# Performance work log

Hardware: AMD Instinct MI355X
Metric: run time of the kernel (lower is better)

Reference implementation:

```python
import jax, jax.numpy as jnp
import numpy as np

B, N, D, H, L = 16, 1024, 256, 128, 2  # batch, nodes, feat dim, gcn_hidden, n_layers (D == 2*H)


def setup_inputs() -> dict:
    key = jax.random.key(0)
    ks = jax.random.split(key, 16)
    inp = {
        "gcn_input": jax.random.normal(ks[0], (B, N, D), jnp.float32),
        # scale adjacencies by 1/N so aggregated features stay O(1)
        "latent_adj": jax.random.uniform(ks[1], (B, N, N), jnp.float32) / N,
        "dep_adj": jax.random.uniform(ks[2], (B, N, N), jnp.float32) / N,
        # stacked per-layer parameters (leading dim L); layers share shapes since D == 2*H
        "refine_gate": jax.random.normal(ks[3], (L, D, 1), jnp.float32) * 0.02,
        "gate_W_in": jax.random.normal(ks[4], (L, D, 1), jnp.float32) * 0.02,
        "gate_b_in": jnp.zeros((L, 1), jnp.float32),
        "gate_W_out": jax.random.normal(ks[5], (L, D, 1), jnp.float32) * 0.02,
        "gate_b_out": jnp.zeros((L, 1), jnp.float32),
        "fc_in_W": jax.random.normal(ks[6], (L, H, D), jnp.float32) * 0.02,
        "fc_in_b": jnp.zeros((L, H), jnp.float32),
        "fc_out_W": jax.random.normal(ks[7], (L, H, D), jnp.float32) * 0.02,
        "fc_out_b": jnp.zeros((L, H), jnp.float32),
        "ln_g": jnp.ones((L, 2 * H), jnp.float32),
        "ln_b": jnp.zeros((L, 2 * H), jnp.float32),
    }
    return inp


def _gcn_layer(x, latent, dep, rg, Wgi, bgi, Wgo, bgo, Wi, bi, Wo, bo, g, b):
    # refine gate blends dependency and latent adjacency per source node
    gate = jax.nn.sigmoid(x @ rg)  # [B,N,1]
    A_in = gate * dep + (1.0 - gate) * latent  # [B,N,N]
    A_out = gate * jnp.swapaxes(dep, -1, -2) + (1.0 - gate) * jnp.swapaxes(latent, -1, -2)
    Ax_in = A_in @ x   # [B,N,D]
    Ax_out = A_out @ x
    # gcn gates (scalar bias added after the gated product, as in torch)
    Ax_in = Ax_in * jax.nn.sigmoid(Ax_in @ Wgi) + bgi
    Ax_out = Ax_out * jax.nn.sigmoid(Ax_out @ Wgo) + bgo
    # rec_fc(Ax) + rec_fc(x): weight applied to sum, bias counted twice (faithful)
    h_in = (Ax_in + x) @ Wi.T + 2.0 * bi   # [B,N,H]
    h_out = (Ax_out + x) @ Wo.T + 2.0 * bo
    h = jnp.concatenate([h_in, h_out], axis=-1)  # [B,N,2H]
    mu = jnp.mean(h, axis=-1, keepdims=True)
    var = jnp.var(h, axis=-1, keepdims=True)
    h = (h - mu) * jax.lax.rsqrt(var + 1e-5) * g + b
    return jax.nn.gelu(h, approximate=False)


def reference(gcn_input, latent_adj, dep_adj, refine_gate, gate_W_in, gate_b_in,
              gate_W_out, gate_b_out, fc_in_W, fc_in_b, fc_out_W, fc_out_b, ln_g, ln_b):
    x = gcn_input
    for l in range(refine_gate.shape[0]):  # small fixed layer count
        x = _gcn_layer(x, latent_adj, dep_adj, refine_gate[l],
                       gate_W_in[l], gate_b_in[l], gate_W_out[l], gate_b_out[l],
                       fc_in_W[l], fc_in_b[l], fc_out_W[l], fc_out_b[l],
                       ln_g[l], ln_b[l])
    return x
```

## Files before the change

### kernel.cpp

```cpp
#include <hip/hip_runtime.h>
#include <hip/hip_bf16.h>
#include <cstdint>

#define B_ 16
#define N_ 1024
#define D_ 256
#define H_ 128

typedef unsigned short u16;
typedef __attribute__((ext_vector_type(8))) short bf16x8;
typedef __attribute__((ext_vector_type(4))) float f32x4;

__device__ __forceinline__ u16 f2bf(float f) {
    union { float f; uint32_t u; } v; v.f = f;
    return (u16)((v.u + 0x7FFFu + ((v.u >> 16) & 1u)) >> 16);
}
__device__ __forceinline__ float bf2f(u16 h) {
    union { uint32_t u; float f; } v; v.u = ((uint32_t)h) << 16;
    return v.f;
}

typedef __attribute__((address_space(3))) void lds_void;
typedef const __attribute__((address_space(1))) void g_void;

__device__ __forceinline__ void gl_lds16(const void* g, void* l) {
    __builtin_amdgcn_global_load_lds((g_void*)g, (lds_void*)l, 16, 0, 0);
}

__device__ __forceinline__ void vm_wait4() { asm volatile("s_waitcnt vmcnt(4)" ::: "memory"); }
__device__ __forceinline__ void vm_wait2() { asm volatile("s_waitcnt vmcnt(2)" ::: "memory"); }
__device__ __forceinline__ void vm_wait0() { asm volatile("s_waitcnt vmcnt(0)" ::: "memory"); }
__device__ __forceinline__ void lgkm0()   { asm volatile("s_waitcnt lgkmcnt(0)" ::: "memory"); }

__global__ __launch_bounds__(256) void k_conv_adj(
    const float* __restrict__ dep, const float* __restrict__ lat,
    u16* __restrict__ depb, u16* __restrict__ latb,
    u16* __restrict__ depTb, u16* __restrict__ latTb)
{
    __shared__ u16 tile[64][64];
    const int bz = blockIdx.z;
    const int b = bz >> 1;
    const float* src = (bz & 1) ? lat : dep;
    u16* dstN = (bz & 1) ? latb : depb;
    u16* dstT = (bz & 1) ? latTb : depTb;
    const int r0 = blockIdx.y * 64, c0 = blockIdx.x * 64;
    const int t = threadIdx.x;
    const int r = t >> 2, cg = (t & 3) * 16;

    const float* srow = src + ((size_t)b * N_ + r0 + r) * N_ + c0 + cg;
    bf16x8 lo, hi;
    {
        const float4 v0 = *(const float4*)(srow);
        const float4 v1 = *(const float4*)(srow + 4);
        const float4 v2 = *(const float4*)(srow + 8);
        const float4 v3 = *(const float4*)(srow + 12);
        lo[0] = (short)f2bf(v0.x); lo[1] = (short)f2bf(v0.y); lo[2] = (short)f2bf(v0.z); lo[3] = (short)f2bf(v0.w);
        lo[4] = (short)f2bf(v1.x); lo[5] = (short)f2bf(v1.y); lo[6] = (short)f2bf(v1.z); lo[7] = (short)f2bf(v1.w);
        hi[0] = (short)f2bf(v2.x); hi[1] = (short)f2bf(v2.y); hi[2] = (short)f2bf(v2.z); hi[3] = (short)f2bf(v2.w);
        hi[4] = (short)f2bf(v3.x); hi[5] = (short)f2bf(v3.y); hi[6] = (short)f2bf(v3.z); hi[7] = (short)f2bf(v3.w);
    }
    u16* nrow = dstN + ((size_t)b * N_ + r0 + r) * N_ + c0 + cg;
    *(bf16x8*)nrow = lo;
    *(bf16x8*)(nrow + 8) = hi;

    const int g0 = (t & 3) * 2;
    const int s = r & 7;
    *(bf16x8*)(&tile[r][((g0    ) ^ s) * 8]) = lo;
    *(bf16x8*)(&tile[r][((g0 + 1) ^ s) * 8]) = hi;
    __syncthreads();

    const int sc = t >> 2, rg2 = (t & 3) * 16;
    bf16x8 o0, o1;
    #pragma unroll
    for (int i = 0; i < 8; ++i) {
        const int R = rg2 + i;
        o0[i] = (short)tile[R][(((sc >> 3) ^ (R & 7)) * 8) + (sc & 7)];
    }
    #pragma unroll
    for (int i = 0; i < 8; ++i) {
        const int R = rg2 + 8 + i;
        o1[i] = (short)tile[R][(((sc >> 3) ^ (R & 7)) * 8) + (sc & 7)];
    }
    u16* dT = dstT + ((size_t)b * N_ + c0 + sc) * N_ + r0 + rg2;
    *(bf16x8*)dT = o0;
    *(bf16x8*)(dT + 8) = o1;
}

__global__ __launch_bounds__(256) void k_gate_xt(
    const float* __restrict__ x, const float* __restrict__ rg,
    float* __restrict__ gate, u16* __restrict__ xT,
    const float* __restrict__ wi, const float* __restrict__ wo,
    u16* __restrict__ wib, u16* __restrict__ wob)
{
    if (blockIdx.y >= B_) {
        const int i = ((blockIdx.y - B_) * 32 + blockIdx.x) * 256 + threadIdx.x;
        wib[i] = f2bf(wi[i]);
        wob[i] = f2bf(wo[i]);
        return;
    }

    __shared__ u16 lx[D_][36];
    __shared__ float srg[D_];
    const int b = blockIdx.y, n0 = blockIdx.x * 32;
    const int t = threadIdx.x;
    srg[t] = rg[t];
    __syncthreads();

    const int r = t >> 3, cg = t & 7;
    const float* xrow = x + ((size_t)b * N_ + n0 + r) * D_;
    float dot = 0.f;
    #pragma unroll
    for (int u = 0; u < 8; ++u) {
        const int c = cg * 32 + u * 4;
        const float4 v = *(const float4*)(xrow + c);
        lx[c][r] = f2bf(v.x); lx[c + 1][r] = f2bf(v.y);
        lx[c + 2][r] = f2bf(v.z); lx[c + 3][r] = f2bf(v.w);
        dot += v.x * srg[c] + v.y * srg[c + 1] + v.z * srg[c + 2] + v.w * srg[c + 3];
    }
    dot += __shfl_down(dot, 4, 8);
    dot += __shfl_down(dot, 2, 8);
    dot += __shfl_down(dot, 1, 8);
    if (cg == 0) gate[(size_t)b * N_ + n0 + r] = 1.f / (1.f + expf(-dot));
    __syncthreads();

    #pragma unroll
    for (int i = 0; i < 8; ++i) {
        const int unit = i * 256 + t;
        const int d = unit >> 3, nch = (unit & 7) * 4;
        ushort4 wv;
        wv.x = lx[d][nch];     wv.y = lx[d][nch + 1];
        wv.z = lx[d][nch + 2]; wv.w = lx[d][nch + 3];
        *(ushort4*)(xT + ((size_t)b * D_ + d) * N_ + n0 + nch) = wv;
    }
}

__global__ __launch_bounds__(512, 2) void k_gemm_ax(
    const u16* __restrict__ depb, const u16* __restrict__ latb,
    const u16* __restrict__ depTb, const u16* __restrict__ latTb,
    const u16* __restrict__ xT,
    const float* __restrict__ gate,
    const float* __restrict__ Wgi, const float* __restrict__ Wgo,
    const float* __restrict__ bgi, const float* __restrict__ bgo,
    const float* __restrict__ xcur,
    u16* __restrict__ axin, u16* __restrict__ axout)
{
    __shared__ __align__(16) char smem[51712];
    u16* const sb = (u16*)smem;
    float* hbuf = (float*)smem;
    float* psum = (float*)(smem + 49152);
    float* sh_s = (float*)(smem + 51200);

    const int bid = blockIdx.x;
    const int logical = (bid & 7) * 32 + (bid >> 3);
    const int b = logical >> 4;
    const int rem = logical & 15;
    const int z = rem >> 3;
    const int m0 = (rem & 7) * 128;

    const u16* A1 = z ? depTb : depb;
    const u16* A2 = z ? latTb : latb;
    const float* Wg = z ? Wgo : Wgi;
    const float bg0 = z ? bgo[0] : bgi[0];
    u16* outp = z ? axout : axin;

    const int t = threadIdx.x;
    const int lane = t & 63;
    const int w = t >> 6;
    const int wr = w >> 2, wc = w & 3;

    const int arow = t >> 2;
    const int akq = t & 3;
    const float gv = gate[(size_t)b * N_ + m0 + arow];
    const u16* gA1 = A1 + ((size_t)b * N_ + m0 + arow) * N_ + akq * 8;
    const u16* gA2 = A2 + ((size_t)b * N_ + m0 + arow) * N_ + akq * 8;
    const int awoff = arow * 32 + ((akq ^ ((arow >> 1) & 3)) << 3);

    const int rl = lane >> 2;
    const int kk = (((lane & 3) ^ ((lane >> 3) & 3)) << 3);
    const u16* gB0 = xT + ((size_t)b * D_ + (w * 2) * 16 + rl) * N_ + kk;
    const u16* gB1 = xT + ((size_t)b * D_ + (w * 2 + 1) * 16 + rl) * N_ + kk;
    const int boff0 = 4096 + (w * 2) * 512;
    const int boff1 = 4096 + (w * 2 + 1) * 512;

    const int mrow = lane & 15;
    const int hi = lane >> 4;
    const int kg = (((lane >> 4) ^ ((mrow >> 1) & 3)) << 3);

    f32x4 acc[4][4];
    const f32x4 fz = {0.f, 0.f, 0.f, 0.f};
    #pragma unroll
    for (int i = 0; i < 4; ++i)
        #pragma unroll
        for (int j = 0; j < 4; ++j) acc[i][j] = fz;

    bf16x8 rA1x, rA2x, rA1y, rA2y;

    auto blend_store = [&](const bf16x8& a1v, const bf16x8& a2v, u16* dst) {
        bf16x8 bl;
        #pragma unroll
        for (int u = 0; u < 8; ++u) {
            const float f1 = bf2f((u16)a1v[u]);
            const float f2 = bf2f((u16)a2v[u]);
            bl[u] = (short)f2bf(f2 + gv * (f1 - f2));
        }
        *(bf16x8*)dst = bl;
    };

    rA1x = *(const bf16x8*)(gA1);       rA2x = *(const bf16x8*)(gA2);
    blend_store(rA1x, rA2x, sb + awoff);
    rA1x = *(const bf16x8*)(gA1 + 32);  rA2x = *(const bf16x8*)(gA2 + 32);
    gl_lds16(gB0, sb + boff0);          gl_lds16(gB1, sb + boff1);
    blend_store(rA1x, rA2x, sb + 12288 + awoff);
    rA1x = *(const bf16x8*)(gA1 + 64);  rA2x = *(const bf16x8*)(gA2 + 64);
    gl_lds16(gB0 + 32, sb + 12288 + boff0); gl_lds16(gB1 + 32, sb + 12288 + boff1);
    vm_wait4();
    lgkm0();
    __builtin_amdgcn_sched_barrier(0);
    __builtin_amdgcn_s_barrier();
    __builtin_amdgcn_sched_barrier(0);

    auto body = [&](int ks, bf16x8& c1, bf16x8& c2, bf16x8& n1, bf16x8& n2) {
        if (ks <= 28) {
            n1 = *(const bf16x8*)(gA1 + (ks + 3) * 32);
            n2 = *(const bf16x8*)(gA2 + (ks + 3) * 32);
        }
        const u16* sA = sb + (ks & 1) * 12288;
        const u16* sBc = sA + 4096;
        bf16x8 a[4], fbv[4];
        #pragma unroll
        for (int mt = 0; mt < 4; ++mt)
            a[mt] = *(const bf16x8*)(sA + (wr * 64 + mt * 16 + mrow) * 32 + kg);
        #pragma unroll
        for (int nt = 0; nt < 4; ++nt)
            fbv[nt] = *(const bf16x8*)(sBc + (wc * 64 + nt * 16 + mrow) * 32 + kg);
        #pragma unroll
        for (int mt = 0; mt < 4; ++mt)
            #pragma unroll
            for (int nt = 0; nt < 4; ++nt)
                acc[mt][nt] = __builtin_amdgcn_mfma_f32_16x16x32_bf16(a[mt], fbv[nt], acc[mt][nt], 0, 0, 0);
        __builtin_amdgcn_sched_barrier(0);
        __builtin_amdgcn_s_barrier();
        __builtin_amdgcn_sched_barrier(0);
        if (ks <= 29) {
            u16* cb = sb + (ks & 1) * 12288;
            blend_store(c1, c2, cb + awoff);
            gl_lds16(gB0 + (ks + 2) * 32, cb + boff0);
            gl_lds16(gB1 + (ks + 2) * 32, cb + boff1);
        }
        if (ks <= 28) vm_wait4();
        else if (ks == 29) vm_wait2();
        else if (ks == 30) vm_wait0();
        lgkm0();
        __builtin_amdgcn_sched_barrier(0);
        __builtin_amdgcn_s_barrier();
        __builtin_amdgcn_sched_barrier(0);
    };

    for (int kp = 0; kp < 16; ++kp) {
        body(2 * kp,     rA1x, rA2x, rA1y, rA2y);
        body(2 * kp + 1, rA1y, rA2y, rA1x, rA2x);
    }
    __syncthreads();

    float wgv[4];
    #pragma unroll
    for (int nt = 0; nt < 4; ++nt) wgv[nt] = Wg[wc * 64 + nt * 16 + mrow];
    #pragma unroll
    for (int mt = 0; mt < 4; ++mt) {
        #pragma unroll
        for (int rr = 0; rr < 4; ++rr) {
            float p = acc[mt][0][rr] * wgv[0] + acc[mt][1][rr] * wgv[1]
                    + acc[mt][2][rr] * wgv[2] + acc[mt][3][rr] * wgv[3];
            p += __shfl_xor(p, 1, 16);
            p += __shfl_xor(p, 2, 16);
            p += __shfl_xor(p, 4, 16);
            p += __shfl_xor(p, 8, 16);
            if (mrow == 0) psum[(wr * 64 + mt * 16 + hi * 4 + rr) * 4 + wc] = p;
        }
    }
    __syncthreads();
    if (t < 128) {
        const float d = psum[t * 4] + psum[t * 4 + 1] + psum[t * 4 + 2] + psum[t * 4 + 3];
        sh_s[t] = 1.f / (1.f + expf(-d));
    }
    __syncthreads();

    #pragma unroll
    for (int p = 0; p < 4; ++p) {
        if (wr == (p >> 1)) {
            #pragma unroll
            for (int mtl = 0; mtl < 2; ++mtl) {
                const int mt = (p & 1) * 2 + mtl;
                #pragma unroll
                for (int nt = 0; nt < 4; ++nt) {
                    const int col = wc * 64 + nt * 16 + mrow;
                    #pragma unroll
                    for (int rr = 0; rr < 4; ++rr) {
                        const int hrow = mtl * 16 + hi * 4 + rr;
                        hbuf[hrow * 260 + col] = acc[mt][nt][rr];
                    }
                }
            }
        }
        __syncthreads();
        {
            const int sr = t >> 4;
            const int sc0 = (t & 15) * 16;
            const int grow = p * 32 + sr;
            const float s = sh_s[grow];
            const size_t gb = ((size_t)b * N_ + m0 + grow) * D_ + sc0;
            const float* xr = xcur + gb;
            u16* orow = outp + gb;
            bf16x8 o0, o1;
            #pragma unroll
            for (int u = 0; u < 8; ++u)
                o0[u] = (short)f2bf(hbuf[sr * 260 + sc0 + u] * s + bg0 + xr[u]);
            #pragma unroll
            for (int u = 0; u < 8; ++u)
                o1[u] = (short)f2bf(hbuf[sr * 260 + sc0 + 8 + u] * s + bg0 + xr[8 + u]);
            *(bf16x8*)orow = o0;
            *(bf16x8*)(orow + 8) = o1;
        }
        __syncthreads();
    }
}

__global__ __launch_bounds__(256, 2) void k_fc_ln(
    const u16* __restrict__ axin, const u16* __restrict__ axout,
    const u16* __restrict__ Wib, const u16* __restrict__ Wob,
    const float* __restrict__ bi, const float* __restrict__ bo,
    const float* __restrict__ lg, const float* __restrict__ lb,
    float* __restrict__ outp)
{
    __shared__ __align__(16) char smem[61696];
    float* hbuf = (float*)smem;
    float* sh_mu = (float*)(smem + 61440);
    float* sh_rs = (float*)(smem + 61568);

    const int b = blockIdx.y, m0 = blockIdx.x * 32;
    const int t = threadIdx.x, lane = t & 63, w = t >> 6;
    const int half = w >> 1, wn = w & 1;

    f32x4 acc[2][4];
    const f32x4 fz = {0.f, 0.f, 0.f, 0.f};
    #pragma unroll
    for (int i = 0; i < 2; ++i)
        #pragma unroll
        for (int j = 0; j < 4; ++j) acc[i][j] = fz;

    const u16* gsrc[5];
    int loff[5];
    const int rl = lane >> 2;
    const int kk = (((lane & 3) ^ ((lane >> 3) & 3)) << 3);
    #pragma unroll
    for (int ci = 0; ci < 5; ++ci) {
        const int c = w * 5 + ci;
        if (c < 4) {
            const int cc = c & 1;
            const int m = cc * 16 + rl;
            const u16* base = (c < 2) ? axin : axout;
            gsrc[ci] = base + ((size_t)b * N_ + m0 + m) * D_ + kk;
            loff[ci] = ((c < 2) ? 0 : 1024) + cc * 512;
        } else {
            const int cc = (c - 4) & 7;
            const int n = cc * 16 + rl;
            const u16* base = (c < 12) ? Wib : Wob;
            gsrc[ci] = base + (size_t)n * D_ + kk;
            loff[ci] = ((c < 12) ? 2048 : 6144) + cc * 512;
        }
    }

    u16* const sb = (u16*)smem;

    #pragma unroll
    for (int ci = 0; ci < 5; ++ci) gl_lds16(gsrc[ci], sb + loff[ci]);
    #pragma unroll
    for (int ci = 0; ci < 5; ++ci) { gl_lds16(gsrc[ci] + 32, sb + 10240 + loff[ci]); gsrc[ci] += 64; }

    const int mrow = lane & 15;
    const int kg = (((lane >> 4) ^ ((mrow >> 1) & 3)) << 3);

    for (int ks = 0; ks < D_ / 32; ++ks) {
        if (ks == 7) vm_wait0(); else { asm volatile("s_waitcnt vmcnt(5)" ::: "memory"); }
        __builtin_amdgcn_s_barrier();
        __builtin_amdgcn_sched_barrier(0);
        if (ks <= 5) {
            u16* nb = sb + ((ks + 2) % 3) * 10240;
            #pragma unroll
            for (int ci = 0; ci < 5; ++ci) { gl_lds16(gsrc[ci], nb + loff[ci]); gsrc[ci] += 32; }
        }
        const u16* cur = sb + (ks % 3) * 10240;
        const u16* sA = cur + (half ? 1024 : 0);
        const u16* sW = cur + 2048 + (half ? 4096 : 0);
        bf16x8 a[2], fb[4];
        #pragma unroll
        for (int mt = 0; mt < 2; ++mt)
            a[mt] = *(const bf16x8*)(sA + (mt * 16 + mrow) * 32 + kg);
        #pragma unroll
        for (int nt = 0; nt < 4; ++nt)
            fb[nt] = *(const bf16x8*)(sW + (wn * 64 + nt * 16 + mrow) * 32 + kg);
        #pragma unroll
        for (int mt = 0; mt < 2; ++mt)
            #pragma unroll
            for (int nt = 0; nt < 4; ++nt)
                acc[mt][nt] = __builtin_amdgcn_mfma_f32_16x16x32_bf16(a[mt], fb[nt], acc[mt][nt], 0, 0, 0);
    }
    __syncthreads();

    const int hi = lane >> 4;
    #pragma unroll
    for (int mt = 0; mt < 2; ++mt)
        #pragma unroll
        for (int nt = 0; nt < 4; ++nt) {
            const int colh = wn * 64 + nt * 16 + mrow;
            const int col = half * 128 + colh;
            const float bias = 2.f * (half ? bo[colh] : bi[colh]);
            #pragma unroll
            for (int rr = 0; rr < 4; ++rr) {
                const int row = mt * 16 + hi * 4 + rr;
                hbuf[row * 260 + col] = acc[mt][nt][rr] + bias;
            }
        }
    __syncthreads();

    {
        const int rr = t >> 3;
        const int c0 = (t & 7) * 32;
        float s = 0.f, ss = 0.f;
        #pragma unroll 8
        for (int u = 0; u < 32; ++u) {
            const float v = hbuf[rr * 260 + c0 + u];
            s += v; ss += v * v;
        }
        s += __shfl_down(s, 4, 8);  ss += __shfl_down(ss, 4, 8);
        s += __shfl_down(s, 2, 8);  ss += __shfl_down(ss, 2, 8);
        s += __shfl_down(s, 1, 8);  ss += __shfl_down(ss, 1, 8);
        if ((t & 7) == 0) {
            const float mu = s * (1.f / 256.f);
            const float var = ss * (1.f / 256.f) - mu * mu;
            sh_mu[rr] = mu;
            sh_rs[rr] = rsqrtf(var + 1e-5f);
        }
    }
    __syncthreads();

    #pragma unroll
    for (int i = 0; i < 16; ++i) {
        const int row = (t >> 7) + i * 2;
        const int c = (t & 127) * 2;
        const float mu = sh_mu[row], rs = sh_rs[row];
        const float2 gg = *(const float2*)(lg + c);
        const float2 bb = *(const float2*)(lb + c);
        const float v0 = (hbuf[row * 260 + c] - mu) * rs * gg.x + bb.x;
        const float v1 = (hbuf[row * 260 + c + 1] - mu) * rs * gg.y + bb.y;
        const float y0 = 0.5f * v0 * (1.f + erff(v0 * 0.70710678118654752f));
        const float y1 = 0.5f * v1 * (1.f + erff(v1 * 0.70710678118654752f));
        const size_t gidx = ((size_t)b * N_ + m0 + row) * D_ + c;
        *(float2*)(outp + gidx) = make_float2(y0, y1);
    }
}

extern "C" void kernel_launch(void* const* d_in, const int* in_sizes, int n_in,
                              void* d_out, int out_size, void* d_ws, size_t ws_size,
                              hipStream_t stream)
{
    (void)in_sizes; (void)n_in; (void)out_size; (void)ws_size;

    const float* x0  = (const float*)d_in[0];
    const float* lat = (const float*)d_in[1];
    const float* dep = (const float*)d_in[2];
    const float* rg  = (const float*)d_in[3];
    const float* Wgi = (const float*)d_in[4];
    const float* bgi = (const float*)d_in[5];
    const float* Wgo = (const float*)d_in[6];
    const float* bgo = (const float*)d_in[7];
    const float* fiW = (const float*)d_in[8];
    const float* fib = (const float*)d_in[9];
    const float* foW = (const float*)d_in[10];
    const float* fob = (const float*)d_in[11];
    const float* lng = (const float*)d_in[12];
    const float* lnb = (const float*)d_in[13];

    char* ws = (char*)d_ws;
    size_t off = 0;
    auto alloc = [&](size_t bytes) {
        char* p = ws + off;
        off += (bytes + 255) & ~(size_t)255;
        return p;
    };
    u16* depb  = (u16*)alloc(2ull * B_ * N_ * N_);
    u16* latb  = (u16*)alloc(2ull * B_ * N_ * N_);
    u16* depTb = (u16*)alloc(2ull * B_ * N_ * N_);
    u16* latTb = (u16*)alloc(2ull * B_ * N_ * N_);
    u16* xT    = (u16*)alloc(2ull * B_ * D_ * N_);
    u16* axin  = (u16*)alloc(2ull * B_ * N_ * D_);
    u16* axout = (u16*)alloc(2ull * B_ * N_ * D_);
    float* gate = (float*)alloc(4ull * B_ * N_);
    float* xbuf = (float*)alloc(4ull * B_ * N_ * D_);
    u16* Wib = (u16*)alloc(2ull * H_ * D_);
    u16* Wob = (u16*)alloc(2ull * H_ * D_);

    k_conv_adj<<<dim3(16, 16, 32), 256, 0, stream>>>(dep, lat, depb, latb, depTb, latTb);

    const float* xcur = x0;
    for (int l = 0; l < 2; ++l) {
        k_gate_xt<<<dim3(32, B_ + 4), 256, 0, stream>>>(
            xcur, rg + l * D_, gate, xT,
            fiW + (size_t)l * H_ * D_, foW + (size_t)l * H_ * D_, Wib, Wob);
        k_gemm_ax<<<dim3(256), 512, 0, stream>>>(
            depb, latb, depTb, latTb, xT, gate,
            Wgi + l * D_, Wgo + l * D_, bgi + l, bgo + l,
            xcur, axin, axout);
        const bool last = (l == 1);
        k_fc_ln<<<dim3(32, B_), 256, 0, stream>>>(
            axin, axout, Wib, Wob,
            fib + l * H_, fob + l * H_,
            lng + l * 2 * H_, lnb + l * 2 * H_,
            last ? (float*)d_out : xbuf);
        xcur = xbuf;
    }
}
```

Before: 321.0 us.

## Read fp32 adjacency directly in A_in GEMM and retile fc+layernorm kernel

The conversion kernel no longer writes non-transposed bf16 copies of dep and latent adjacency. The A_in half of the aggregation GEMM now loads the fp32 originals and converts them on the fly during the blend, while the transposed half keeps its bf16 copies. This saves the bf16 write and the later re-read of two large matrices, but the A_in path now reads twice as many bytes per layer, and the tail of that GEMM now waits at a different vmcnt depth. Separately, the fc+layernorm kernel moves to 512 threads with 64-row tiles, double-buffered LDS, and in-register row statistics via shuffles, and its grid is swizzled.

After: 336.6 us. +4.9%, slower.

```diff
diff --git a/kernel.cpp b/kernel.cpp
--- a/kernel.cpp
+++ b/kernel.cpp
@@ -9,7 +9,10 @@
 
 typedef unsigned short u16;
 typedef __attribute__((ext_vector_type(8))) short bf16x8;
+typedef __attribute__((ext_vector_type(4))) short bf16x4;
 typedef __attribute__((ext_vector_type(4))) float f32x4;
+
+template<int V> struct IC { static constexpr int value = V; };
 
 __device__ __forceinline__ u16 f2bf(float f) {
     union { float f; uint32_t u; } v; v.f = f;
@@ -27,21 +30,21 @@
     __builtin_amdgcn_global_load_lds((g_void*)g, (lds_void*)l, 16, 0, 0);
 }
 
-__device__ __forceinline__ void vm_wait4() { asm volatile("s_waitcnt vmcnt(4)" ::: "memory"); }
+__device__ __forceinline__ void vm_wait6() { asm volatile("s_waitcnt vmcnt(6)" ::: "memory"); }
+__device__ __forceinline__ void vm_wait3() { asm volatile("s_waitcnt vmcnt(3)" ::: "memory"); }
 __device__ __forceinline__ void vm_wait2() { asm volatile("s_waitcnt vmcnt(2)" ::: "memory"); }
 __device__ __forceinline__ void vm_wait0() { asm volatile("s_waitcnt vmcnt(0)" ::: "memory"); }
 __device__ __forceinline__ void lgkm0()   { asm volatile("s_waitcnt lgkmcnt(0)" ::: "memory"); }
+__device__ __forceinline__ void schedb()  { __builtin_amdgcn_sched_barrier(0); }
 
 __global__ __launch_bounds__(256) void k_conv_adj(
     const float* __restrict__ dep, const float* __restrict__ lat,
-    u16* __restrict__ depb, u16* __restrict__ latb,
     u16* __restrict__ depTb, u16* __restrict__ latTb)
 {
     __shared__ u16 tile[64][64];
     const int bz = blockIdx.z;
     const int b = bz >> 1;
     const float* src = (bz & 1) ? lat : dep;
-    u16* dstN = (bz & 1) ? latb : depb;
     u16* dstT = (bz & 1) ? latTb : depTb;
     const int r0 = blockIdx.y * 64, c0 = blockIdx.x * 64;
     const int t = threadIdx.x;
@@ -59,9 +62,6 @@
         hi[0] = (short)f2bf(v2.x); hi[1] = (short)f2bf(v2.y); hi[2] = (short)f2bf(v2.z); hi[3] = (short)f2bf(v2.w);
         hi[4] = (short)f2bf(v3.x); hi[5] = (short)f2bf(v3.y); hi[6] = (short)f2bf(v3.z); hi[7] = (short)f2bf(v3.w);
     }
-    u16* nrow = dstN + ((size_t)b * N_ + r0 + r) * N_ + c0 + cg;
-    *(bf16x8*)nrow = lo;
-    *(bf16x8*)(nrow + 8) = hi;
 
     const int g0 = (t & 3) * 2;
     const int s = r & 7;
@@ -135,7 +135,7 @@
 }
 
 __global__ __launch_bounds__(512, 2) void k_gemm_ax(
-    const u16* __restrict__ depb, const u16* __restrict__ latb,
+    const float* __restrict__ depf, const float* __restrict__ latf,
     const u16* __restrict__ depTb, const u16* __restrict__ latTb,
     const u16* __restrict__ xT,
     const float* __restrict__ gate,
@@ -157,8 +157,6 @@
     const int z = rem >> 3;
     const int m0 = (rem & 7) * 128;
 
-    const u16* A1 = z ? depTb : depb;
-    const u16* A2 = z ? latTb : latb;
     const float* Wg = z ? Wgo : Wgi;
     const float bg0 = z ? bgo[0] : bgi[0];
     u16* outp = z ? axout : axin;
@@ -171,9 +169,11 @@
     const int arow = t >> 2;
     const int akq = t & 3;
     const float gv = gate[(size_t)b * N_ + m0 + arow];
-    const u16* gA1 = A1 + ((size_t)b * N_ + m0 + arow) * N_ + akq * 8;
-    const u16* gA2 = A2 + ((size_t)b * N_ + m0 + arow) * N_ + akq * 8;
     const int awoff = arow * 32 + ((akq ^ ((arow >> 1) & 3)) << 3);
+    const float* gD = depf + ((size_t)b * N_ + m0 + arow) * N_ + akq * 8;
+    const float* gL = latf + ((size_t)b * N_ + m0 + arow) * N_ + akq * 8;
+    const u16* gT1 = depTb + ((size_t)b * N_ + m0 + arow) * N_ + akq * 8;
+    const u16* gT2 = latTb + ((size_t)b * N_ + m0 + arow) * N_ + akq * 8;
 
     const int rl = lane >> 2;
     const int kk = (((lane & 3) ^ ((lane >> 3) & 3)) << 3);
@@ -193,73 +193,103 @@
         #pragma unroll
         for (int j = 0; j < 4; ++j) acc[i][j] = fz;
 
-    bf16x8 rA1x, rA2x, rA1y, rA2y;
-
-    auto blend_store = [&](const bf16x8& a1v, const bf16x8& a2v, u16* dst) {
-        bf16x8 bl;
-        #pragma unroll
-        for (int u = 0; u < 8; ++u) {
-            const float f1 = bf2f((u16)a1v[u]);
-            const float f2 = bf2f((u16)a2v[u]);
-            bl[u] = (short)f2bf(f2 + gv * (f1 - f2));
-        }
-        *(bf16x8*)dst = bl;
+    struct RegsF { float4 d0, d1, l0, l1; };
+    struct RegsH { bf16x4 a0, a1, b0, b1; };
+
+    auto run = [&](auto zc) {
+        constexpr int Z = decltype(zc)::value;
+
+        auto LOAD = [&](auto& r, int ks) {
+            if constexpr (Z == 0) {
+                r.d0 = *(const float4*)(gD + ks * 32);
+                r.d1 = *(const float4*)(gD + ks * 32 + 4);
+                r.l0 = *(const float4*)(gL + ks * 32);
+                r.l1 = *(const float4*)(gL + ks * 32 + 4);
+            } else {
+                r.a0 = *(const bf16x4*)(gT1 + ks * 32);
+                r.a1 = *(const bf16x4*)(gT1 + ks * 32 + 4);
+                r.b0 = *(const bf16x4*)(gT2 + ks * 32);
+                r.b1 = *(const bf16x4*)(gT2 + ks * 32 + 4);
+            }
+        };
+        auto BLEND = [&](const auto& r, u16* dst) {
+            bf16x8 bl;
+            if constexpr (Z == 0) {
+                bl[0] = (short)f2bf(r.l0.x + gv * (r.d0.x - r.l0.x));
+                bl[1] = (short)f2bf(r.l0.y + gv * (r.d0.y - r.l0.y));
+                bl[2] = (short)f2bf(r.l0.z + gv * (r.d0.z - r.l0.z));
+                bl[3] = (short)f2bf(r.l0.w + gv * (r.d0.w - r.l0.w));
+                bl[4] = (short)f2bf(r.l1.x + gv * (r.d1.x - r.l1.x));
+                bl[5] = (short)f2bf(r.l1.y + gv * (r.d1.y - r.l1.y));
+                bl[6] = (short)f2bf(r.l1.z + gv * (r.d1.z - r.l1.z));
+                bl[7] = (short)f2bf(r.l1.w + gv * (r.d1.w - r.l1.w));
+            } else {
+                #pragma unroll
+                for (int u = 0; u < 4; ++u) {
+                    const float f1 = bf2f((u16)r.a0[u]);
+                    const float f2 = bf2f((u16)r.b0[u]);
+                    bl[u] = (short)f2bf(f2 + gv * (f1 - f2));
+                }
+                #pragma unroll
+                for (int u = 0; u < 4; ++u) {
+                    const float f1 = bf2f((u16)r.a1[u]);
+                    const float f2 = bf2f((u16)r.b1[u]);
+                    bl[4 + u] = (short)f2bf(f2 + gv * (f1 - f2));
+                }
+            }
+            *(bf16x8*)dst = bl;
+        };
+
+        auto body = [&](int ks, auto& c, auto& n) {
+            if (ks <= 28) LOAD(n, ks + 3);
+            const u16* sA = sb + (ks & 1) * 12288;
+            const u16* sBc = sA + 4096;
+            bf16x8 a[4], fbv[4];
+            #pragma unroll
+            for (int mt = 0; mt < 4; ++mt)
+                a[mt] = *(const bf16x8*)(sA + (wr * 64 + mt * 16 + mrow) * 32 + kg);
+            #pragma unroll
+            for (int nt = 0; nt < 4; ++nt)
+                fbv[nt] = *(const bf16x8*)(sBc + (wc * 64 + nt * 16 + mrow) * 32 + kg);
+            #pragma unroll
+            for (int mt = 0; mt < 4; ++mt)
+                #pragma unroll
+                for (int nt = 0; nt < 4; ++nt)
+                    acc[mt][nt] = __builtin_amdgcn_mfma_f32_16x16x32_bf16(a[mt], fbv[nt], acc[mt][nt], 0, 0, 0);
+            schedb();
+            __builtin_amdgcn_s_barrier();
+            schedb();
+            if (ks <= 29) {
+                u16* cb = sb + (ks & 1) * 12288;
+                BLEND(c, cb + awoff);
+                gl_lds16(gB0 + (ks + 2) * 32, cb + boff0);
+                gl_lds16(gB1 + (ks + 2) * 32, cb + boff1);
+            }
+            if (ks <= 28) vm_wait6();
+            else if (ks == 29) vm_wait2();
+            else if (ks == 30) vm_wait0();
+            lgkm0();
+            schedb();
+            __builtin_amdgcn_s_barrier();
+            schedb();
+        };
+
+        typename std::conditional<Z == 0, RegsF, RegsH>::type x, y;
+        LOAD(x, 0); BLEND(x, sb + awoff);
+        LOAD(y, 1); BLEND(y, sb + 12288 + awoff);
+        LOAD(x, 2);
+        gl_lds16(gB0, sb + boff0);          gl_lds16(gB1, sb + boff1);
+        gl_lds16(gB0 + 32, sb + 12288 + boff0); gl_lds16(gB1 + 32, sb + 12288 + boff1);
+        vm_wait2();
+        lgkm0();
+        schedb(); __builtin_amdgcn_s_barrier(); schedb();
+
+        for (int kp = 0; kp < 16; ++kp) {
+            body(2 * kp, x, y);
+            body(2 * kp + 1, y, x);
+        }
     };
-
-    rA1x = *(const bf16x8*)(gA1);       rA2x = *(const bf16x8*)(gA2);
-    blend_store(rA1x, rA2x, sb + awoff);
-    rA1x = *(const bf16x8*)(gA1 + 32);  rA2x = *(const bf16x8*)(gA2 + 32);
-    gl_lds16(gB0, sb + boff0);          gl_lds16(gB1, sb + boff1);
-    blend_store(rA1x, rA2x, sb + 12288 + awoff);
-    rA1x = *(const bf16x8*)(gA1 + 64);  rA2x = *(const bf16x8*)(gA2 + 64);
-    gl_lds16(gB0 + 32, sb + 12288 + boff0); gl_lds16(gB1 + 32, sb + 12288 + boff1);
-    vm_wait4();
-    lgkm0();
-    __builtin_amdgcn_sched_barrier(0);
-    __builtin_amdgcn_s_barrier();
-    __builtin_amdgcn_sched_barrier(0);
-
-    auto body = [&](int ks, bf16x8& c1, bf16x8& c2, bf16x8& n1, bf16x8& n2) {
-        if (ks <= 28) {
-            n1 = *(const bf16x8*)(gA1 + (ks + 3) * 32);
-            n2 = *(const bf16x8*)(gA2 + (ks + 3) * 32);
-        }
-        const u16* sA = sb + (ks & 1) * 12288;
-        const u16* sBc = sA + 4096;
-        bf16x8 a[4], fbv[4];
-        #pragma unroll
-        for (int mt = 0; mt < 4; ++mt)
-            a[mt] = *(const bf16x8*)(sA + (wr * 64 + mt * 16 + mrow) * 32 + kg);
-        #pragma unroll
-        for (int nt = 0; nt < 4; ++nt)
-            fbv[nt] = *(const bf16x8*)(sBc + (wc * 64 + nt * 16 + mrow) * 32 + kg);
-        #pragma unroll
-        for (int mt = 0; mt < 4; ++mt)
-            #pragma unroll
-            for (int nt = 0; nt < 4; ++nt)
-                acc[mt][nt] = __builtin_amdgcn_mfma_f32_16x16x32_bf16(a[mt], fbv[nt], acc[mt][nt], 0, 0, 0);
-        __builtin_amdgcn_sched_barrier(0);
-        __builtin_amdgcn_s_barrier();
-        __builtin_amdgcn_sched_barrier(0);
-        if (ks <= 29) {
-            u16* cb = sb + (ks & 1) * 12288;
-            blend_store(c1, c2, cb + awoff);
-            gl_lds16(gB0 + (ks + 2) * 32, cb + boff0);
-            gl_lds16(gB1 + (ks + 2) * 32, cb + boff1);
-        }
-        if (ks <= 28) vm_wait4();
-        else if (ks == 29) vm_wait2();
-        else if (ks == 30) vm_wait0();
-        lgkm0();
-        __builtin_amdgcn_sched_barrier(0);
-        __builtin_amdgcn_s_barrier();
-        __builtin_amdgcn_sched_barrier(0);
-    };
-
-    for (int kp = 0; kp < 16; ++kp) {
-        body(2 * kp,     rA1x, rA2x, rA1y, rA2y);
-        body(2 * kp + 1, rA1y, rA2y, rA1x, rA2x);
-    }
+    if (z == 0) run(IC<0>()); else run(IC<1>());
     __syncthreads();
 
     float wgv[4];
@@ -325,21 +355,51 @@
     }
 }
 
-__global__ __launch_bounds__(256, 2) void k_fc_ln(
+__global__ __launch_bounds__(512, 2) void k_fc_ln(
     const u16* __restrict__ axin, const u16* __restrict__ axout,
     const u16* __restrict__ Wib, const u16* __restrict__ Wob,
     const float* __restrict__ bi, const float* __restrict__ bo,
     const float* __restrict__ lg, const float* __restrict__ lb,
     float* __restrict__ outp)
 {
-    __shared__ __align__(16) char smem[61696];
+    __shared__ __align__(16) char smem[51712];
+    u16* const sb = (u16*)smem;
     float* hbuf = (float*)smem;
-    float* sh_mu = (float*)(smem + 61440);
-    float* sh_rs = (float*)(smem + 61568);
-
-    const int b = blockIdx.y, m0 = blockIdx.x * 32;
+    float* psum = (float*)(smem + 49152);
+    float* sh_mu = (float*)(smem + 51200);
+    float* sh_rs = (float*)(smem + 51456);
+
+    const int bid = blockIdx.x;
+    const int logical = (bid & 7) * 32 + (bid >> 3);
+    const int b = logical >> 4;
+    const int m0 = (logical & 15) * 64;
+
     const int t = threadIdx.x, lane = t & 63, w = t >> 6;
-    const int half = w >> 1, wn = w & 1;
+    const int wr = w >> 2, wc = w & 3;
+    const int half = wc >> 1;
+
+    const int rl = lane >> 2;
+    const int kk = (((lane & 3) ^ ((lane >> 3) & 3)) << 3);
+
+    const u16* gsrc[3];
+    int loff[3];
+    #pragma unroll
+    for (int ci = 0; ci < 3; ++ci) {
+        const int c = w * 3 + ci;
+        if (c < 4) {
+            gsrc[ci] = axin + ((size_t)b * N_ + m0 + c * 16 + rl) * D_ + kk;
+            loff[ci] = c * 512;
+        } else if (c < 8) {
+            gsrc[ci] = axout + ((size_t)b * N_ + m0 + (c - 4) * 16 + rl) * D_ + kk;
+            loff[ci] = 2048 + (c - 4) * 512;
+        } else {
+            const int cw = c - 8;
+            const u16* base = (cw < 8) ? (Wib + (size_t)(cw * 16 + rl) * D_)
+                                       : (Wob + (size_t)((cw - 8) * 16 + rl) * D_);
+            gsrc[ci] = base + kk;
+            loff[ci] = 4096 + cw * 512;
+        }
+    }
 
     f32x4 acc[2][4];
     const f32x4 fz = {0.f, 0.f, 0.f, 0.f};
@@ -348,115 +408,127 @@
         #pragma unroll
         for (int j = 0; j < 4; ++j) acc[i][j] = fz;
 
-    const u16* gsrc[5];
-    int loff[5];
-    const int rl = lane >> 2;
-    const int kk = (((lane & 3) ^ ((lane >> 3) & 3)) << 3);
-    #pragma unroll
-    for (int ci = 0; ci < 5; ++ci) {
-        const int c = w * 5 + ci;
-        if (c < 4) {
-            const int cc = c & 1;
-            const int m = cc * 16 + rl;
-            const u16* base = (c < 2) ? axin : axout;
-            gsrc[ci] = base + ((size_t)b * N_ + m0 + m) * D_ + kk;
-            loff[ci] = ((c < 2) ? 0 : 1024) + cc * 512;
-        } else {
-            const int cc = (c - 4) & 7;
-            const int n = cc * 16 + rl;
-            const u16* base = (c < 12) ? Wib : Wob;
-            gsrc[ci] = base + (size_t)n * D_ + kk;
-            loff[ci] = ((c < 12) ? 2048 : 6144) + cc * 512;
-        }
-    }
-
-    u16* const sb = (u16*)smem;
-
-    #pragma unroll
-    for (int ci = 0; ci < 5; ++ci) gl_lds16(gsrc[ci], sb + loff[ci]);
-    #pragma unroll
-    for (int ci = 0; ci < 5; ++ci) { gl_lds16(gsrc[ci] + 32, sb + 10240 + loff[ci]); gsrc[ci] += 64; }
+    #pragma unroll
+    for (int ci = 0; ci < 3; ++ci) gl_lds16(gsrc[ci], sb + loff[ci]);
+    #pragma unroll
+    for (int ci = 0; ci < 3; ++ci) gl_lds16(gsrc[ci] + 32, sb + 12288 + loff[ci]);
+    vm_wait3();
+    lgkm0();
+    schedb(); __builtin_amdgcn_s_barrier(); schedb();
 
     const int mrow = lane & 15;
+    const int hi = lane >> 4;
     const int kg = (((lane >> 4) ^ ((mrow >> 1) & 3)) << 3);
 
-    for (int ks = 0; ks < D_ / 32; ++ks) {
-        if (ks == 7) vm_wait0(); else { asm volatile("s_waitcnt vmcnt(5)" ::: "memory"); }
+    for (int ks = 0; ks < 8; ++ks) {
+        const u16* cur = sb + (ks & 1) * 12288;
+        const u16* sA = cur + (half ? 2048 : 0);
+        const u16* sW = cur + 4096;
+        bf16x8 a[2], fbv[4];
+        #pragma unroll
+        for (int mt = 0; mt < 2; ++mt)
+            a[mt] = *(const bf16x8*)(sA + (wr * 32 + mt * 16 + mrow) * 32 + kg);
+        #pragma unroll
+        for (int nt = 0; nt < 4; ++nt)
+            fbv[nt] = *(const bf16x8*)(sW + (wc * 64 + nt * 16 + mrow) * 32 + kg);
+        #pragma unroll
+        for (int mt = 0; mt < 2; ++mt)
+            #pragma unroll
+            for (int nt = 0; nt < 4; ++nt)
+                acc[mt][nt] = __builtin_amdgcn_mfma_f32_16x16x32_bf16(a[mt], fbv[nt], acc[mt][nt], 0, 0, 0);
+        schedb();
         __builtin_amdgcn_s_barrier();
-        __builtin_amdgcn_sched_barrier(0);
+        schedb();
         if (ks <= 5) {
-            u16* nb = sb + ((ks + 2) % 3) * 10240;
-            #pragma unroll
-            for (int ci = 0; ci < 5; ++ci) { gl_lds16(gsrc[ci], nb + loff[ci]); gsrc[ci] += 32; }
-        }
-        const u16* cur = sb + (ks % 3) * 10240;
-        const u16* sA = cur + (half ? 1024 : 0);
-        const u16* sW = cur + 2048 + (half ? 4096 : 0);
-        bf16x8 a[2], fb[4];
-        #pragma unroll
-        for (int mt = 0; mt < 2; ++mt)
-            a[mt] = *(const bf16x8*)(sA + (mt * 16 + mrow) * 32 + kg);
-        #pragma unroll
-        for (int nt = 0; nt < 4; ++nt)
-            fb[nt] = *(const bf16x8*)(sW + (wn * 64 + nt * 16 + mrow) * 32 + kg);
-        #pragma unroll
-        for (int mt = 0; mt < 2; ++mt)
-            #pragma unroll
-            for (int nt = 0; nt < 4; ++nt)
-                acc[mt][nt] = __builtin_amdgcn_mfma_f32_16x16x32_bf16(a[mt], fb[nt], acc[mt][nt], 0, 0, 0);
-    }
-    __syncthreads();
-
-    const int hi = lane >> 4;
+            u16* nb = sb + (ks & 1) * 12288;
+            #pragma unroll
+            for (int ci = 0; ci < 3; ++ci) gl_lds16(gsrc[ci] + (ks + 2) * 32, nb + loff[ci]);
+        }
+        if (ks <= 5) vm_wait3();
+        else if (ks == 6) vm_wait0();
+        lgkm0();
+        schedb();
+        __builtin_amdgcn_s_barrier();
+        schedb();
+    }
+    __syncthreads();
+
+    float bc[4];
+    #pragma unroll
+    for (int nt = 0; nt < 4; ++nt) {
+        const int colh = wc * 64 + nt * 16 + mrow;
+        bc[nt] = 2.f * (colh < 128 ? bi[colh] : bo[colh - 128]);
+    }
     #pragma unroll
     for (int mt = 0; mt < 2; ++mt)
         #pragma unroll
-        for (int nt = 0; nt < 4; ++nt) {
-            const int colh = wn * 64 + nt * 16 + mrow;
-            const int col = half * 128 + colh;
-            const float bias = 2.f * (half ? bo[colh] : bi[colh]);
-            #pragma unroll
-            for (int rr = 0; rr < 4; ++rr) {
-                const int row = mt * 16 + hi * 4 + rr;
-                hbuf[row * 260 + col] = acc[mt][nt][rr] + bias;
-            }
-        }
-    __syncthreads();
-
-    {
-        const int rr = t >> 3;
-        const int c0 = (t & 7) * 32;
-        float s = 0.f, ss = 0.f;
-        #pragma unroll 8
-        for (int u = 0; u < 32; ++u) {
-            const float v = hbuf[rr * 260 + c0 + u];
-            s += v; ss += v * v;
-        }
-        s += __shfl_down(s, 4, 8);  ss += __shfl_down(ss, 4, 8);
-        s += __shfl_down(s, 2, 8);  ss += __shfl_down(ss, 2, 8);
-        s += __shfl_down(s, 1, 8);  ss += __shfl_down(ss, 1, 8);
-        if ((t & 7) == 0) {
-            const float mu = s * (1.f / 256.f);
-            const float var = ss * (1.f / 256.f) - mu * mu;
-            sh_mu[rr] = mu;
-            sh_rs[rr] = rsqrtf(var + 1e-5f);
-        }
-    }
-    __syncthreads();
-
-    #pragma unroll
-    for (int i = 0; i < 16; ++i) {
-        const int row = (t >> 7) + i * 2;
-        const int c = (t & 127) * 2;
-        const float mu = sh_mu[row], rs = sh_rs[row];
-        const float2 gg = *(const float2*)(lg + c);
-        const float2 bb = *(const float2*)(lb + c);
-        const float v0 = (hbuf[row * 260 + c] - mu) * rs * gg.x + bb.x;
-        const float v1 = (hbuf[row * 260 + c + 1] - mu) * rs * gg.y + bb.y;
-        const float y0 = 0.5f * v0 * (1.f + erff(v0 * 0.70710678118654752f));
-        const float y1 = 0.5f * v1 * (1.f + erff(v1 * 0.70710678118654752f));
-        const size_t gidx = ((size_t)b * N_ + m0 + row) * D_ + c;
-        *(float2*)(outp + gidx) = make_float2(y0, y1);
+        for (int rr = 0; rr < 4; ++rr) {
+            const int lrow = wr * 32 + mt * 16 + hi * 4 + rr;
+            float s = 0.f, ss = 0.f;
+            #pragma unroll
+            for (int nt = 0; nt < 4; ++nt) {
+                const float v = acc[mt][nt][rr] + bc[nt];
+                s += v; ss += v * v;
+            }
+            s += __shfl_xor(s, 1, 16);  ss += __shfl_xor(ss, 1, 16);
+            s += __shfl_xor(s, 2, 16);  ss += __shfl_xor(ss, 2, 16);
+            s += __shfl_xor(s, 4, 16);  ss += __shfl_xor(ss, 4, 16);
+            s += __shfl_xor(s, 8, 16);  ss += __shfl_xor(ss, 8, 16);
+            if (mrow == 0) {
+                psum[lrow * 8 + wc * 2] = s;
+                psum[lrow * 8 + wc * 2 + 1] = ss;
+            }
+        }
+    __syncthreads();
+    if (t < 64) {
+        const float s = psum[t * 8] + psum[t * 8 + 2] + psum[t * 8 + 4] + psum[t * 8 + 6];
+        const float ss = psum[t * 8 + 1] + psum[t * 8 + 3] + psum[t * 8 + 5] + psum[t * 8 + 7];
+        const float mu = s * (1.f / 256.f);
+        const float var = ss * (1.f / 256.f) - mu * mu;
+        sh_mu[t] = mu;
+        sh_rs[t] = rsqrtf(var + 1e-5f);
+    }
+    __syncthreads();
+
+    #pragma unroll
+    for (int p = 0; p < 2; ++p) {
+        if (wr == p) {
+            #pragma unroll
+            for (int mt = 0; mt < 2; ++mt)
+                #pragma unroll
+                for (int nt = 0; nt < 4; ++nt) {
+                    const int col = wc * 64 + nt * 16 + mrow;
+                    #pragma unroll
+                    for (int rr = 0; rr < 4; ++rr) {
+                        const int hrow = mt * 16 + hi * 4 + rr;
+                        hbuf[hrow * 260 + col] = acc[mt][nt][rr] + bc[nt];
+                    }
+                }
+        }
+        __syncthreads();
+        {
+            const int sr = t >> 4;
+            const int sc0 = (t & 15) * 16;
+            const int grow = p * 32 + sr;
+            const float mu = sh_mu[grow], rs = sh_rs[grow];
+            float* orow = outp + ((size_t)b * N_ + m0 + grow) * D_ + sc0;
+            #pragma unroll
+            for (int q = 0; q < 4; ++q) {
+                const float4 gg = *(const float4*)(lg + sc0 + q * 4);
+                const float4 bb = *(const float4*)(lb + sc0 + q * 4);
+                float4 o;
+                const float v0 = (hbuf[sr * 260 + sc0 + q * 4    ] - mu) * rs * gg.x + bb.x;
+                const float v1 = (hbuf[sr * 260 + sc0 + q * 4 + 1] - mu) * rs * gg.y + bb.y;
+                const float v2 = (hbuf[sr * 260 + sc0 + q * 4 + 2] - mu) * rs * gg.z + bb.z;
+                const float v3 = (hbuf[sr * 260 + sc0 + q * 4 + 3] - mu) * rs * gg.w + bb.w;
+                o.x = 0.5f * v0 * (1.f + erff(v0 * 0.70710678118654752f));
+                o.y = 0.5f * v1 * (1.f + erff(v1 * 0.70710678118654752f));
+                o.z = 0.5f * v2 * (1.f + erff(v2 * 0.70710678118654752f));
+                o.w = 0.5f * v3 * (1.f + erff(v3 * 0.70710678118654752f));
+                *(float4*)(orow + q * 4) = o;
+            }
+        }
+        __syncthreads();
     }
 }
 
@@ -488,8 +560,6 @@
         off += (bytes + 255) & ~(size_t)255;
         return p;
     };
-    u16* depb  = (u16*)alloc(2ull * B_ * N_ * N_);
-    u16* latb  = (u16*)alloc(2ull * B_ * N_ * N_);
     u16* depTb = (u16*)alloc(2ull * B_ * N_ * N_);
     u16* latTb = (u16*)alloc(2ull * B_ * N_ * N_);
     u16* xT    = (u16*)alloc(2ull * B_ * D_ * N_);
@@ -500,7 +570,7 @@
     u16* Wib = (u16*)alloc(2ull * H_ * D_);
     u16* Wob = (u16*)alloc(2ull * H_ * D_);
 
-    k_conv_adj<<<dim3(16, 16, 32), 256, 0, stream>>>(dep, lat, depb, latb, depTb, latTb);
+    k_conv_adj<<<dim3(16, 16, 32), 256, 0, stream>>>(dep, lat, depTb, latTb);
 
     const float* xcur = x0;
     for (int l = 0; l < 2; ++l) {
@@ -508,11 +578,11 @@
             xcur, rg + l * D_, gate, xT,
             fiW + (size_t)l * H_ * D_, foW + (size_t)l * H_ * D_, Wib, Wob);
         k_gemm_ax<<<dim3(256), 512, 0, stream>>>(
-            depb, latb, depTb, latTb, xT, gate,
+            dep, lat, depTb, latTb, xT, gate,
             Wgi + l * D_, Wgo + l * D_, bgi + l, bgo + l,
             xcur, axin, axout);
         const bool last = (l == 1);
-        k_fc_ln<<<dim3(32, B_), 256, 0, stream>>>(
+        k_fc_ln<<<dim3(256), 512, 0, stream>>>(
             axin, axout, Wib, Wob,
             fib + l * H_, fob + l * H_,
             lng + l * 2 * H_, lnb + l * 2 * H_,
```
